# Kernel optimization log

Hardware: AMD Instinct MI355X
Metric: run time of the kernel (lower is better)

## Reference

```python
import jax, jax.numpy as jnp
import numpy as np

B, T, D, H = 64, 1024, 128, 256
TIME_UNIT = 1.0
FORGET_BIAS = 1.0


def setup_inputs() -> dict:
    key = jax.random.key(0)
    ks = jax.random.split(key, 12)
    x = jax.random.normal(ks[0], (B, T, D), jnp.float32)
    # True = missing observation (matches torch semantics: masked_fill(mask, 0))
    mask = jax.random.bernoulli(ks[1], 0.2, (B, T, D))
    # strictly increasing timestamps with deltas in [0.5, 1.5)
    dt = jax.random.uniform(ks[2], (B, T), jnp.float32, 0.5, 1.5)
    time_step = jnp.cumsum(dt, axis=1)
    # init_time one unit before first observation -> first delta = 1 (avoids log(0))
    init_time = (time_step[:, 0] - 1.0)[None, :]  # [1, B]
    s = 1.0 / np.sqrt(H)
    w_ih = jax.random.uniform(ks[3], (3 * H, D), jnp.float32, -s, s)
    w_hh = jax.random.uniform(ks[4], (3 * H, H), jnp.float32, -s, s)
    b_ih = jax.random.uniform(ks[5], (3 * H,), jnp.float32, -s, s)
    # _reset_parameters fills bias_ih[H:2H] with forget_bias (update-gate slice)
    b_ih = b_ih.at[H:2 * H].set(FORGET_BIAS)
    b_hh = jax.random.uniform(ks[6], (3 * H,), jnp.float32, -s, s)
    # decay params: small positive so relu is active and exp(-.) is non-degenerate
    input_decay_w = jax.random.uniform(ks[7], (D, D), jnp.float32, 0.0, 0.02)
    input_decay_b = jax.random.uniform(ks[8], (D,), jnp.float32, 0.0, 0.1)
    hidden_decay_w = jax.random.uniform(ks[9], (H, 1), jnp.float32, 0.0, 0.5)
    hidden_decay_b = jax.random.uniform(ks[10], (H,), jnp.float32, 0.0, 0.1)
    return dict(input=x, mask=mask, time_step=time_step, init_time=init_time,
                w_ih=w_ih, w_hh=w_hh, b_ih=b_ih, b_hh=b_hh,
                input_decay_w=input_decay_w, input_decay_b=input_decay_b,
                hidden_decay_w=hidden_decay_w, hidden_decay_b=hidden_decay_b)


def _process_missing(x, mask, time_delta, idw, idb):
    # scan computing forward-filled input and per-feature time since last obs
    def step(carry, xs):
        prev_x, prev_td = carry
        m, xt, tdt = xs
        prev_x = jnp.where(m, prev_x, xt)          # keep prev where missing
        prev_td = prev_td + tdt
        out = (prev_x, prev_td)
        new_td = jnp.where(m, prev_td, 0.0)        # reset where observed
        return (prev_x, new_td), out

    td3 = jnp.broadcast_to(time_delta[:, :, None], x.shape)  # [B,T,D]
    init = (jnp.zeros_like(x[:, 0]), jnp.zeros_like(x[:, 0]))
    xs = (jnp.swapaxes(mask, 0, 1), jnp.swapaxes(x, 0, 1), jnp.swapaxes(td3, 0, 1))
    _, (ffill, idelta) = jax.lax.scan(step, init, xs)
    ffill = jnp.swapaxes(ffill, 0, 1)              # [B,T,D]
    idelta = jnp.swapaxes(idelta, 0, 1)
    # NOTE: faithful to torch source, which divides by count of *missing* entries
    denom = jnp.clip(mask.astype(x.dtype).sum(axis=1), 1.0, None)
    input_mean = (jnp.where(mask, 0.0, x).sum(axis=1) / denom)[:, None, :]
    idelta = jnp.clip(TIME_UNIT * (idelta - 1.0), 0.0, 1000.0)
    fill_w = jnp.exp(-jax.nn.relu(idelta @ idw.T + idb))
    filled = ffill * fill_w + (1.0 - fill_w) * input_mean
    return jnp.where(mask, filled, x)


def reference(input, mask, time_step, init_time, w_ih, w_hh, b_ih, b_hh,
              input_decay_w, input_decay_b, hidden_decay_w, hidden_decay_b):
    # time deltas (forward direction, init_time[0] is fw init time)
    ts = jnp.concatenate([init_time[0][:, None], time_step], axis=1)
    time_delta = ts[:, 1:] - ts[:, :-1]            # [B,T]
    x = _process_missing(input, mask, time_delta, input_decay_w, input_decay_b)
    tdl = jnp.log(jnp.clip(TIME_UNIT * time_delta, 0.0, 1000.0))  # [B,T]

    hdw = hidden_decay_w[:, 0]                     # [H]

    def cell(h, xs):
        xt, tdt = xs                               # xt [B,D], tdt [B]
        decay = jnp.exp(-jax.nn.relu(tdt[:, None] * hdw[None, :] + hidden_decay_b))
        h = h * decay
        gi = xt @ w_ih.T + b_ih                    # [B,3H]
        gh = h @ w_hh.T + b_hh
        ir, iz, inn = jnp.split(gi, 3, axis=1)
        hr, hz, hn = jnp.split(gh, 3, axis=1)
        r = jax.nn.sigmoid(ir + hr)
        z = jax.nn.sigmoid(iz + hz)
        n = jnp.tanh(inn + r * hn)
        h = (1.0 - z) * n + z * h
        return h, h

    h0 = jnp.zeros((x.shape[0], hidden_decay_b.shape[0]), x.dtype)
    h_last, hidden = jax.lax.scan(cell, h0, (jnp.swapaxes(x, 0, 1), tdl.T))
    hidden = jnp.swapaxes(hidden, 0, 1)            # [B,T,H]
    return hidden, h_last[None]                    # state unsqueezed on dim 0
```

## Files before the change

kernel.cpp:

```cpp
#include <hip/hip_runtime.h>

constexpr int B = 64, T = 1024, D = 128, H = 256;
constexpr int NG = 64;
constexpr int GK = 4;
constexpr int UO = 64;
constexpr int CS = 40;

__device__ __forceinline__ float sigmoidf_(float v) {
    return 1.f / (1.f + __expf(-v));
}
__device__ __forceinline__ float tanhf_(float v) {
    float e2 = __expf(2.f * v);
    return 1.f - 2.f / (e2 + 1.f);
}

__global__ __launch_bounds__(64) void prep_scan(
    const float* __restrict__ x, const int* __restrict__ mask,
    const float* __restrict__ ts, const float* __restrict__ it0,
    float* __restrict__ ffill, float* __restrict__ idelta,
    float* __restrict__ mean, float* __restrict__ tdlv)
{
    const int b = blockIdx.x;
    const int d = blockIdx.y * 64 + threadIdx.x;
    float prev_x = 0.f, prev_td = 0.f, osum = 0.f, mcnt = 0.f;
    float prev_ts = it0[b];
    const int baseT = b * T;
    constexpr int U = 16;
    for (int t0 = 0; t0 < T; t0 += U) {
        float xv[U]; int mv[U]; float tsv[U];
        #pragma unroll
        for (int u = 0; u < U; ++u) {
            const int idx = (baseT + t0 + u) * D + d;
            xv[u] = x[idx];
            mv[u] = mask[idx];
        }
        #pragma unroll
        for (int u = 0; u < U; ++u) tsv[u] = ts[baseT + t0 + u];
        #pragma unroll
        for (int u = 0; u < U; ++u) {
            const float td = tsv[u] - prev_ts;
            prev_ts = tsv[u];
            const int idx = (baseT + t0 + u) * D + d;
            if (!mv[u]) { prev_x = xv[u]; osum += xv[u]; } else { mcnt += 1.f; }
            prev_td += td;
            ffill[idx]  = prev_x;
            idelta[idx] = prev_td;
            if (!mv[u]) prev_td = 0.f;
            if (d == 0) tdlv[baseT + t0 + u] = logf(fminf(fmaxf(td, 0.f), 1000.f));
        }
    }
    mean[b * D + d] = osum / fmaxf(mcnt, 1.f);
}

constexpr int ROWS = 64;
__global__ __launch_bounds__(256) void fill_kernel(
    const float* __restrict__ x, const int* __restrict__ mask,
    const float* __restrict__ ffill, const float* __restrict__ idelta,
    const float* __restrict__ mean, const float* __restrict__ idw,
    const float* __restrict__ idb, float* __restrict__ xf)
{
    __shared__ float widw[128 * 129];
    __shared__ float ide[2][128];
    const int tid = threadIdx.x;
    for (int i = tid; i < 128 * 128; i += 256)
        widw[(i >> 7) * 129 + (i & 127)] = idw[i];
    __syncthreads();
    const int p = tid >> 7, d = tid & 127;
    const float bias = idb[d];
    const int row0 = blockIdx.x * ROWS;
    for (int r = 0; r < ROWS; r += 2) {
        const int rowp = row0 + r + p;
        const int idx = rowp * D + d;
        ide[p][d] = fminf(fmaxf(idelta[idx] - 1.f, 0.f), 1000.f);
        __syncthreads();
        float acc = bias;
        #pragma unroll
        for (int k = 0; k < 128; ++k)
            acc = fmaf(ide[p][k], widw[d * 129 + k], acc);
        float fw = __expf(-fmaxf(acc, 0.f));
        float filled = ffill[idx] * fw + (1.f - fw) * mean[(rowp >> 10) * D + d];
        xf[idx] = mask[idx] ? filled : x[idx];
        __syncthreads();
    }
}

__global__ __launch_bounds__(512, 2) void rnn_kernel(
    const float* __restrict__ xf, const float* __restrict__ tdlv,
    const float* __restrict__ w_ih, const float* __restrict__ w_hh,
    const float* __restrict__ b_ih, const float* __restrict__ b_hh,
    const float* __restrict__ hdw, const float* __restrict__ hdb,
    unsigned long long* __restrict__ hx, float* __restrict__ out)
{
    const int tid = threadIdx.x;
    const int g  = blockIdx.x & (NG - 1);
    const int kb = blockIdx.x >> 6;
    const int u_loc = tid >> 3;
    const int kc = tid & 7;
    const int row = kb * UO + u_loc;
    const int b = g;

    float whr[32], whz[32], whn[32];
    #pragma unroll
    for (int j = 0; j < 32; ++j) {
        whr[j] = w_hh[(row        ) * H + kc * 32 + j];
        whz[j] = w_hh[(row +     H) * H + kc * 32 + j];
        whn[j] = w_hh[(row + 2 * H) * H + kc * 32 + j];
    }
    float wir[16], wiz[16], win_[16];
    #pragma unroll
    for (int j = 0; j < 16; ++j) {
        wir[j]  = w_ih[(row        ) * D + kc * 16 + j];
        wiz[j]  = w_ih[(row +     H) * D + kc * 16 + j];
        win_[j] = w_ih[(row + 2 * H) * D + kc * 16 + j];
    }
    const bool stager = (tid < H);
    const bool ownk = stager && ((tid >> 6) == kb);
    const float hdwk = stager ? hdw[tid] : 0.f;
    const float hdbk = stager ? hdb[tid] : 0.f;
    const float hdwo = hdw[row];
    const float hdbo = hdb[row];
    float br = 0.f, bz = 0.f, bnx = 0.f, bnh = 0.f;
    if (kc == 0) {
        br  = b_ih[row] + b_hh[row];
        bz  = b_ih[H + row] + b_hh[H + row];
        bnx = b_ih[2 * H + row];
        bnh = b_hh[2 * H + row];
    }

    __shared__ float hdec[2][8 * CS];
    for (int i = tid; i < 2 * 8 * CS; i += 512)
        ((float*)hdec)[i] = 0.f;
    __syncthreads();

    const float* tdlb = tdlv + b * T;

    for (int t = 0; t < T; ++t) {
        const int par = t & 1;

        const bool need = (t > 0) && stager && !ownk;
        const unsigned long long* slot =
            hx + (size_t)((t - 1) & 1) * (B * H) + b * H + tid;
        unsigned long long v = 0;
        if (need)
            v = __hip_atomic_load(slot, __ATOMIC_RELAXED, __HIP_MEMORY_SCOPE_AGENT);

        const float4* xp4 = (const float4*)(xf + (size_t)(b * T + t) * D + kc * 16);
        float a0 = 0.f, a1 = 0.f, a2 = 0.f;
        #pragma unroll
        for (int i = 0; i < 4; ++i) {
            float4 xq = xp4[i];
            a0 = fmaf(wir[4*i  ], xq.x, a0); a1 = fmaf(wiz[4*i  ], xq.x, a1); a2 = fmaf(win_[4*i  ], xq.x, a2);
            a0 = fmaf(wir[4*i+1], xq.y, a0); a1 = fmaf(wiz[4*i+1], xq.y, a1); a2 = fmaf(win_[4*i+1], xq.y, a2);
            a0 = fmaf(wir[4*i+2], xq.z, a0); a1 = fmaf(wiz[4*i+2], xq.z, a1); a2 = fmaf(win_[4*i+2], xq.z, a2);
            a0 = fmaf(wir[4*i+3], xq.w, a0); a1 = fmaf(wiz[4*i+3], xq.w, a1); a2 = fmaf(win_[4*i+3], xq.w, a2);
        }

        if (need) {
            while ((unsigned)(v >> 32) != (unsigned)t)
                v = __hip_atomic_load(slot, __ATOMIC_RELAXED, __HIP_MEMORY_SCOPE_AGENT);
            float hv = __uint_as_float((unsigned)v);
            float dec = __expf(-fmaxf(tdlb[t] * hdwk + hdbk, 0.f));
            hdec[par][(tid >> 5) * CS + (tid & 31)] = hv * dec;
        }
        __syncthreads();

        float a3 = 0.f;
        const float4* hp4 = (const float4*)(&hdec[par][kc * CS]);
        #pragma unroll
        for (int i = 0; i < 8; ++i) {
            float4 hq = hp4[i];
            a0 = fmaf(whr[4*i  ], hq.x, a0); a1 = fmaf(whz[4*i  ], hq.x, a1); a3 = fmaf(whn[4*i  ], hq.x, a3);
            a0 = fmaf(whr[4*i+1], hq.y, a0); a1 = fmaf(whz[4*i+1], hq.y, a1); a3 = fmaf(whn[4*i+1], hq.y, a3);
            a0 = fmaf(whr[4*i+2], hq.z, a0); a1 = fmaf(whz[4*i+2], hq.z, a1); a3 = fmaf(whn[4*i+2], hq.z, a3);
            a0 = fmaf(whr[4*i+3], hq.w, a0); a1 = fmaf(whz[4*i+3], hq.w, a1); a3 = fmaf(whn[4*i+3], hq.w, a3);
        }

        #pragma unroll
        for (int m = 1; m < 8; m <<= 1) {
            a0 += __shfl_xor(a0, m, 64);
            a1 += __shfl_xor(a1, m, 64);
            a2 += __shfl_xor(a2, m, 64);
            a3 += __shfl_xor(a3, m, 64);
        }

        if (kc == 0) {
            float hd = hdec[par][(row >> 5) * CS + (row & 31)];
            float r = sigmoidf_(a0 + br);
            float z = sigmoidf_(a1 + bz);
            float n = tanhf_(a2 + bnx + r * (a3 + bnh));
            float hnew = (1.f - z) * n + z * hd;
            __hip_atomic_store(hx + (size_t)par * (B * H) + b * H + row,
                               (((unsigned long long)(unsigned)(t + 1)) << 32) |
                               (unsigned long long)__float_as_uint(hnew),
                               __ATOMIC_RELAXED, __HIP_MEMORY_SCOPE_AGENT);
            if (t + 1 < T) {
                float dec = __expf(-fmaxf(tdlb[t + 1] * hdwo + hdbo, 0.f));
                hdec[par ^ 1][(row >> 5) * CS + (row & 31)] = hnew * dec;
            }
            out[(size_t)(b * T + t) * H + row] = hnew;
            if (t == T - 1)
                out[(size_t)B * T * H + b * H + row] = hnew;
        }
    }
}

extern "C" void kernel_launch(void* const* d_in, const int* in_sizes, int n_in,
                              void* d_out, int out_size, void* d_ws, size_t ws_size,
                              hipStream_t stream) {
    (void)in_sizes; (void)n_in; (void)out_size; (void)ws_size;
    const float* x    = (const float*)d_in[0];
    const int*   mask = (const int*)d_in[1];
    const float* ts   = (const float*)d_in[2];
    const float* it0  = (const float*)d_in[3];
    const float* w_ih = (const float*)d_in[4];
    const float* w_hh = (const float*)d_in[5];
    const float* b_ih = (const float*)d_in[6];
    const float* b_hh = (const float*)d_in[7];
    const float* idw  = (const float*)d_in[8];
    const float* idb  = (const float*)d_in[9];
    const float* hdw  = (const float*)d_in[10];
    const float* hdb  = (const float*)d_in[11];
    float* out = (float*)d_out;

    char* ws = (char*)d_ws;
    float* xf   = (float*)(ws);
    float* tdlv = (float*)(ws + 33554432);
    float* mean = (float*)(ws + 33816576);
    unsigned long long* hx = (unsigned long long*)(ws + 33849344);

    float* ffill  = out;
    float* idelta = out + (size_t)B * T * D;

    hipMemsetAsync(hx, 0, (size_t)(2 * B * H) * 8, stream);

    prep_scan<<<dim3(B, 2), 64, 0, stream>>>(x, mask, ts, it0, ffill, idelta, mean, tdlv);
    fill_kernel<<<(B * T) / ROWS, 256, 0, stream>>>(x, mask, ffill, idelta, mean, idw, idb, xf);
    rnn_kernel<<<NG * GK, 512, 0, stream>>>(xf, tdlv, w_ih, w_hh, b_ih, b_hh, hdw, hdb,
                                            hx, out);
}
```

Baseline: 1.879 ms.

## Move RNN weights from registers to LDS as packed bf16

The recurrent and input weights move out of per-thread registers (144 floats) into shared memory, stored as bf16 pairs packed into uint4 and unpacked with shifts during the FMAs. The launch-bounds occupancy hint of 2 blocks per CU is dropped. The aim is to relieve register pressure, which may have caused spills or limited scheduling, at the cost of LDS reads on every timestep, extra unpack instructions, and reduced weight precision (bf16 rounding) that could break the accuracy tolerance.

Result: slower. 2.414 ms (+28.5%).

```diff
diff --git a/kernel.cpp b/kernel.cpp
--- a/kernel.cpp
+++ b/kernel.cpp
@@ -13,6 +13,20 @@
     float e2 = __expf(2.f * v);
     return 1.f - 2.f / (e2 + 1.f);
 }
+__device__ __forceinline__ unsigned bfpack(float f0, float f1) {
+    unsigned a = __float_as_uint(f0), b = __float_as_uint(f1);
+    unsigned ra = (a + 0x7fffu + ((a >> 16) & 1u)) >> 16;
+    unsigned rb = (b + 0x7fffu + ((b >> 16) & 1u)) >> 16;
+    return (ra & 0xffffu) | (rb << 16);
+}
+__device__ __forceinline__ float blo(unsigned w) { return __uint_as_float(w << 16); }
+__device__ __forceinline__ float bhi(unsigned w) { return __uint_as_float(w & 0xffff0000u); }
+
+#define FMA8(acc, W, xa, xb) do { \
+    acc = fmaf(blo(W.x), xa.x, acc); acc = fmaf(bhi(W.x), xa.y, acc); \
+    acc = fmaf(blo(W.y), xa.z, acc); acc = fmaf(bhi(W.y), xa.w, acc); \
+    acc = fmaf(blo(W.z), xb.x, acc); acc = fmaf(bhi(W.z), xb.y, acc); \
+    acc = fmaf(blo(W.w), xb.z, acc); acc = fmaf(bhi(W.w), xb.w, acc); } while (0)
 
 __global__ __launch_bounds__(64) void prep_scan(
     const float* __restrict__ x, const int* __restrict__ mask,
@@ -29,24 +43,24 @@
     for (int t0 = 0; t0 < T; t0 += U) {
         float xv[U]; int mv[U]; float tsv[U];
         #pragma unroll
-        for (int u = 0; u < U; ++u) {
-            const int idx = (baseT + t0 + u) * D + d;
-            xv[u] = x[idx];
-            mv[u] = mask[idx];
-        }
-        #pragma unroll
-        for (int u = 0; u < U; ++u) tsv[u] = ts[baseT + t0 + u];
-        #pragma unroll
-        for (int u = 0; u < U; ++u) {
-            const float td = tsv[u] - prev_ts;
-            prev_ts = tsv[u];
-            const int idx = (baseT + t0 + u) * D + d;
-            if (!mv[u]) { prev_x = xv[u]; osum += xv[u]; } else { mcnt += 1.f; }
+        for (int uu = 0; uu < U; ++uu) {
+            const int idx = (baseT + t0 + uu) * D + d;
+            xv[uu] = x[idx];
+            mv[uu] = mask[idx];
+        }
+        #pragma unroll
+        for (int uu = 0; uu < U; ++uu) tsv[uu] = ts[baseT + t0 + uu];
+        #pragma unroll
+        for (int uu = 0; uu < U; ++uu) {
+            const float td = tsv[uu] - prev_ts;
+            prev_ts = tsv[uu];
+            const int idx = (baseT + t0 + uu) * D + d;
+            if (!mv[uu]) { prev_x = xv[uu]; osum += xv[uu]; } else { mcnt += 1.f; }
             prev_td += td;
             ffill[idx]  = prev_x;
             idelta[idx] = prev_td;
-            if (!mv[u]) prev_td = 0.f;
-            if (d == 0) tdlv[baseT + t0 + u] = logf(fminf(fmaxf(td, 0.f), 1000.f));
+            if (!mv[uu]) prev_td = 0.f;
+            if (d == 0) tdlv[baseT + t0 + uu] = logf(fminf(fmaxf(td, 0.f), 1000.f));
         }
     }
     mean[b * D + d] = osum / fmaxf(mcnt, 1.f);
@@ -84,7 +98,7 @@
     }
 }
 
-__global__ __launch_bounds__(512, 2) void rnn_kernel(
+__global__ __launch_bounds__(512) void rnn_kernel(
     const float* __restrict__ xf, const float* __restrict__ tdlv,
     const float* __restrict__ w_ih, const float* __restrict__ w_hh,
     const float* __restrict__ b_ih, const float* __restrict__ b_hh,
@@ -99,20 +113,36 @@
     const int row = kb * UO + u_loc;
     const int b = g;
 
-    float whr[32], whz[32], whn[32];
+    __shared__ unsigned wlds[18 * 512 * 4];
+    __shared__ float hdec[2][8 * CS];
+
     #pragma unroll
-    for (int j = 0; j < 32; ++j) {
-        whr[j] = w_hh[(row        ) * H + kc * 32 + j];
-        whz[j] = w_hh[(row +     H) * H + kc * 32 + j];
-        whn[j] = w_hh[(row + 2 * H) * H + kc * 32 + j];
-    }
-    float wir[16], wiz[16], win_[16];
+    for (int gg = 0; gg < 3; ++gg)
+        #pragma unroll
+        for (int jc = 0; jc < 4; ++jc) {
+            const float* src = &w_hh[(size_t)(row + gg * H) * H + kc * 32 + jc * 8];
+            float4 f0 = *(const float4*)src;
+            float4 f1 = *(const float4*)(src + 4);
+            uint4 p;
+            p.x = bfpack(f0.x, f0.y); p.y = bfpack(f0.z, f0.w);
+            p.z = bfpack(f1.x, f1.y); p.w = bfpack(f1.z, f1.w);
+            *(uint4*)&wlds[((gg * 4 + jc) * 512 + tid) * 4] = p;
+        }
     #pragma unroll
-    for (int j = 0; j < 16; ++j) {
-        wir[j]  = w_ih[(row        ) * D + kc * 16 + j];
-        wiz[j]  = w_ih[(row +     H) * D + kc * 16 + j];
-        win_[j] = w_ih[(row + 2 * H) * D + kc * 16 + j];
-    }
+    for (int gg = 0; gg < 3; ++gg)
+        #pragma unroll
+        for (int jc = 0; jc < 2; ++jc) {
+            const float* src = &w_ih[(size_t)(row + gg * H) * D + kc * 16 + jc * 8];
+            float4 f0 = *(const float4*)src;
+            float4 f1 = *(const float4*)(src + 4);
+            uint4 p;
+            p.x = bfpack(f0.x, f0.y); p.y = bfpack(f0.z, f0.w);
+            p.z = bfpack(f1.x, f1.y); p.w = bfpack(f1.z, f1.w);
+            *(uint4*)&wlds[((12 + gg * 2 + jc) * 512 + tid) * 4] = p;
+        }
+    for (int i = tid; i < 2 * 8 * CS; i += 512)
+        ((float*)hdec)[i] = 0.f;
+
     const bool stager = (tid < H);
     const bool ownk = stager && ((tid >> 6) == kb);
     const float hdwk = stager ? hdw[tid] : 0.f;
@@ -126,10 +156,6 @@
         bnx = b_ih[2 * H + row];
         bnh = b_hh[2 * H + row];
     }
-
-    __shared__ float hdec[2][8 * CS];
-    for (int i = tid; i < 2 * 8 * CS; i += 512)
-        ((float*)hdec)[i] = 0.f;
     __syncthreads();
 
     const float* tdlb = tdlv + b * T;
@@ -145,14 +171,16 @@
             v = __hip_atomic_load(slot, __ATOMIC_RELAXED, __HIP_MEMORY_SCOPE_AGENT);
 
         const float4* xp4 = (const float4*)(xf + (size_t)(b * T + t) * D + kc * 16);
-        float a0 = 0.f, a1 = 0.f, a2 = 0.f;
-        #pragma unroll
-        for (int i = 0; i < 4; ++i) {
-            float4 xq = xp4[i];
-            a0 = fmaf(wir[4*i  ], xq.x, a0); a1 = fmaf(wiz[4*i  ], xq.x, a1); a2 = fmaf(win_[4*i  ], xq.x, a2);
-            a0 = fmaf(wir[4*i+1], xq.y, a0); a1 = fmaf(wiz[4*i+1], xq.y, a1); a2 = fmaf(win_[4*i+1], xq.y, a2);
-            a0 = fmaf(wir[4*i+2], xq.z, a0); a1 = fmaf(wiz[4*i+2], xq.z, a1); a2 = fmaf(win_[4*i+2], xq.z, a2);
-            a0 = fmaf(wir[4*i+3], xq.w, a0); a1 = fmaf(wiz[4*i+3], xq.w, a1); a2 = fmaf(win_[4*i+3], xq.w, a2);
+        float a0 = 0.f, a1 = 0.f, a2 = 0.f, a3 = 0.f;
+        #pragma unroll
+        for (int jc = 0; jc < 2; ++jc) {
+            float4 x0 = xp4[jc * 2], x1 = xp4[jc * 2 + 1];
+            uint4 wr = *(const uint4*)&wlds[((12 + 0 * 2 + jc) * 512 + tid) * 4];
+            uint4 wz = *(const uint4*)&wlds[((12 + 1 * 2 + jc) * 512 + tid) * 4];
+            uint4 wn = *(const uint4*)&wlds[((12 + 2 * 2 + jc) * 512 + tid) * 4];
+            FMA8(a0, wr, x0, x1);
+            FMA8(a1, wz, x0, x1);
+            FMA8(a2, wn, x0, x1);
         }
 
         if (need) {
@@ -164,15 +192,17 @@
         }
         __syncthreads();
 
-        float a3 = 0.f;
-        const float4* hp4 = (const float4*)(&hdec[par][kc * CS]);
-        #pragma unroll
-        for (int i = 0; i < 8; ++i) {
-            float4 hq = hp4[i];
-            a0 = fmaf(whr[4*i  ], hq.x, a0); a1 = fmaf(whz[4*i  ], hq.x, a1); a3 = fmaf(whn[4*i  ], hq.x, a3);
-            a0 = fmaf(whr[4*i+1], hq.y, a0); a1 = fmaf(whz[4*i+1], hq.y, a1); a3 = fmaf(whn[4*i+1], hq.y, a3);
-            a0 = fmaf(whr[4*i+2], hq.z, a0); a1 = fmaf(whz[4*i+2], hq.z, a1); a3 = fmaf(whn[4*i+2], hq.z, a3);
-            a0 = fmaf(whr[4*i+3], hq.w, a0); a1 = fmaf(whz[4*i+3], hq.w, a1); a3 = fmaf(whn[4*i+3], hq.w, a3);
+        const float* hbase = &hdec[par][kc * CS];
+        #pragma unroll
+        for (int jc = 0; jc < 4; ++jc) {
+            float4 h0 = *(const float4*)(hbase + jc * 8);
+            float4 h1 = *(const float4*)(hbase + jc * 8 + 4);
+            uint4 wr = *(const uint4*)&wlds[((0 * 4 + jc) * 512 + tid) * 4];
+            uint4 wz = *(const uint4*)&wlds[((1 * 4 + jc) * 512 + tid) * 4];
+            uint4 wn = *(const uint4*)&wlds[((2 * 4 + jc) * 512 + tid) * 4];
+            FMA8(a0, wr, h0, h1);
+            FMA8(a1, wz, h0, h1);
+            FMA8(a3, wn, h0, h1);
         }
 
         #pragma unroll
```
